# Kernel tuning notes

Measured on AMD Instinct MI355X. Metric: run time of the kernel, lower is better.

Reference implementation:

```python
import jax, jax.numpy as jnp
import numpy as np

B, S, D = 4, 2048, 1024
H = 4096          # adapter hidden dim
E = 4             # number of adapters / experts


def setup_inputs() -> dict:
    key = jax.random.key(0)
    ks = jax.random.split(key, 7)
    sd = 1.0 / np.sqrt(D)
    sh = 1.0 / np.sqrt(H)
    return {
        "x":  jax.random.normal(ks[0], (B, S, D), dtype=jnp.float32),
        "Wr": jax.random.uniform(ks[1], (D, E), minval=-sd, maxval=sd, dtype=jnp.float32),
        "br": jax.random.uniform(ks[2], (E,), minval=-sd, maxval=sd, dtype=jnp.float32),
        "W1": jax.random.uniform(ks[3], (E, D, H), minval=-sd, maxval=sd, dtype=jnp.float32),
        "b1": jax.random.uniform(ks[4], (E, H), minval=-sd, maxval=sd, dtype=jnp.float32),
        "W2": jax.random.uniform(ks[5], (E, H, D), minval=-sh, maxval=sh, dtype=jnp.float32),
        "b2": jax.random.uniform(ks[6], (E, D), minval=-sh, maxval=sh, dtype=jnp.float32),
    }


def reference(x, Wr, br, W1, b1, W2, b2):
    # Flatten tokens: (N, D)
    xf = x.reshape(-1, D)
    N = xf.shape[0]

    # Top-1 router (route_type='none' -> router input is x itself)
    logits = xf @ Wr + br                      # (N, E)
    probs = jax.nn.softmax(logits, axis=-1)    # (N, E)
    gate_idx = jnp.argmax(probs, axis=-1)      # (N,) int
    gate_val = jnp.max(probs, axis=-1)         # (N,)

    # Run every expert adapter densely (E small), then select per token.
    h = jnp.einsum('nd,edh->enh', xf, W1) + b1[:, None, :]   # (E, N, H)
    h = jax.nn.silu(h)
    eo = jnp.einsum('enh,ehd->end', h, W2) + b2[:, None, :]  # (E, N, D)

    sel = eo[gate_idx, jnp.arange(N)]          # (N, D) per-token expert output
    out = sel * gate_val[:, None]              # is_scale_prob=True scaling
    return out.reshape(B, S, D)
```

## Files before the change

### kernel.cpp

```cpp
#include <hip/hip_runtime.h>

#define DN 8192
#define DD 1024
#define DH 4096
#define DE 4
#define SLOTS (DN + 512)

typedef unsigned short u16;
typedef float f32x4 __attribute__((ext_vector_type(4)));
typedef __bf16 bf16x8 __attribute__((ext_vector_type(8)));
typedef u16 u16x2 __attribute__((ext_vector_type(2)));
typedef u16 u16x4 __attribute__((ext_vector_type(4)));

__device__ __forceinline__ u16 f2b(float f) {
  union { float f; unsigned u; } v; v.f = f;
  return (u16)((v.u + 0x7FFFu + ((v.u >> 16) & 1u)) >> 16);
}

__device__ __forceinline__ void gl_lds16(const u16* g, u16* l) {
  __builtin_amdgcn_global_load_lds((const __attribute__((address_space(1))) void*)g,
                                   (__attribute__((address_space(3))) void*)l, 16, 0, 0);
}

__global__ __launch_bounds__(256) void router_k(const float* __restrict__ x,
    const float* __restrict__ Wr, const float* __restrict__ br,
    float* __restrict__ gval, int* __restrict__ gidx, int* __restrict__ gpos,
    int* __restrict__ counts, u16* __restrict__ xb)
{
  const int tid = blockIdx.x * 256 + threadIdx.x;
  const int n = tid >> 6, lane = tid & 63;
  const float* xr = x + (size_t)n * DD;
  double a0 = 0., a1 = 0., a2 = 0., a3 = 0.;
#pragma unroll
  for (int k = 0; k < DD / 64; ++k) {
    const int d = lane + k * 64;
    const float xv = xr[d];
    const f32x4 w = *(const f32x4*)&Wr[d * 4];
    a0 += (double)xv * w[0]; a1 += (double)xv * w[1];
    a2 += (double)xv * w[2]; a3 += (double)xv * w[3];
    xb[(size_t)n * DD + d] = f2b(xv);
  }
#pragma unroll
  for (int off = 32; off; off >>= 1) {
    a0 += __shfl_xor(a0, off);
    a1 += __shfl_xor(a1, off);
    a2 += __shfl_xor(a2, off);
    a3 += __shfl_xor(a3, off);
  }
  if (lane == 0) {
    const double l0 = a0 + br[0], l1 = a1 + br[1], l2 = a2 + br[2], l3 = a3 + br[3];
    int bi = 0; double bm = l0;
    if (l1 > bm) { bm = l1; bi = 1; }
    if (l2 > bm) { bm = l2; bi = 2; }
    if (l3 > bm) { bm = l3; bi = 3; }
    const float s = __expf((float)(l0 - bm)) + __expf((float)(l1 - bm)) +
                    __expf((float)(l2 - bm)) + __expf((float)(l3 - bm));
    gval[n] = 1.0f / s;
    gidx[n] = bi;
    gpos[n] = atomicAdd(&counts[bi], 1);
  }
}

__global__ void offsets_k(const int* __restrict__ counts, int* __restrict__ offs) {
  if (threadIdx.x == 0 && blockIdx.x == 0) {
    int o = 0;
#pragma unroll
    for (int e = 0; e < DE; ++e) { offs[e] = o; o += (counts[e] + 127) & ~127; }
    offs[DE] = o;
  }
}

__global__ __launch_bounds__(256) void scatter_k(const int* __restrict__ gidx,
    const int* __restrict__ gpos, const int* __restrict__ offs, int* __restrict__ tlist) {
  const int n = blockIdx.x * 256 + threadIdx.x;
  tlist[offs[gidx[n]] + gpos[n]] = n;
}

__global__ __launch_bounds__(256) void transpose_conv(const float* __restrict__ in,
    u16* __restrict__ out, int R, int C)
{
  __shared__ u16 t[64][66];
  const int r0 = blockIdx.x * 64, c0 = blockIdx.y * 64;
  const size_t mo = (size_t)blockIdx.z * R * C;
  const int tid = threadIdx.x;
  const int i = tid >> 4, j0 = (tid & 15) * 4;
#pragma unroll
  for (int k = 0; k < 4; ++k) {
    const int row = k * 16 + i;
    const f32x4 v = *(const f32x4*)&in[mo + (size_t)(r0 + row) * C + c0 + j0];
    u16x2 u01; u01[0] = f2b(v[0]); u01[1] = f2b(v[1]);
    u16x2 u23; u23[0] = f2b(v[2]); u23[1] = f2b(v[3]);
    *(u16x2*)&t[row][j0] = u01;
    *(u16x2*)&t[row][j0 + 2] = u23;
  }
  __syncthreads();
#pragma unroll
  for (int k = 0; k < 4; ++k) {
    const int p = k * 16 + i;
    u16x4 u;
    u[0] = t[j0 + 0][p]; u[1] = t[j0 + 1][p]; u[2] = t[j0 + 2][p]; u[3] = t[j0 + 3][p];
    *(u16x4*)&out[mo + (size_t)(c0 + p) * R + r0 + j0] = u;
  }
}

__global__ __launch_bounds__(256) void gemm1_k(const u16* __restrict__ xb,
    const u16* __restrict__ w1t, const float* __restrict__ b1,
    const int* __restrict__ tlist, const int* __restrict__ offs, u16* __restrict__ hb)
{
  __shared__ u16 As[4][128][8];
  __shared__ u16 Bs[4][128][8];
  const int row0 = blockIdx.x * 128;
  if (row0 >= offs[DE]) return;
  int e = 0;
  if (row0 >= offs[1]) e = 1;
  if (row0 >= offs[2]) e = 2;
  if (row0 >= offs[3]) e = 3;
  const int h0 = blockIdx.y * 128;
  const int tid = threadIdx.x;
  const int wid = tid >> 6, lane = tid & 63;

  int tA0 = tlist[row0 + lane];
  int tA1 = tlist[row0 + 64 + lane];
  if (tA0 < 0) tA0 = 0;
  if (tA1 < 0) tA1 = 0;
  const u16* pa0 = xb + (size_t)tA0 * DD + wid * 8;
  const u16* pa1 = xb + (size_t)tA1 * DD + wid * 8;
  const u16* pb0 = w1t + (size_t)e * DH * DD + (size_t)(h0 + lane) * DD + wid * 8;
  const u16* pb1 = w1t + (size_t)e * DH * DD + (size_t)(h0 + 64 + lane) * DD + wid * 8;
  u16* lA0 = &As[wid][0][0];
  u16* lA1 = &As[wid][64][0];
  u16* lB0 = &Bs[wid][0][0];
  u16* lB1 = &Bs[wid][64][0];

  const int wr = (wid >> 1) * 64, wc = (wid & 1) * 64;
  const int fr = lane & 15, fq = lane >> 4;

  f32x4 acc[4][4];
#pragma unroll
  for (int m = 0; m < 4; ++m)
#pragma unroll
    for (int n = 0; n < 4; ++n) acc[m][n] = (f32x4)(0.f);

  for (int ks = 0; ks < DD / 32; ++ks) {
    gl_lds16(pa0, lA0); gl_lds16(pa1, lA1);
    gl_lds16(pb0, lB0); gl_lds16(pb1, lB1);
    pa0 += 32; pa1 += 32; pb0 += 32; pb1 += 32;
    __syncthreads();
    bf16x8 af[4], bfv[4];
#pragma unroll
    for (int m = 0; m < 4; ++m) af[m] = *(const bf16x8*)&As[fq][wr + m * 16 + fr][0];
#pragma unroll
    for (int n = 0; n < 4; ++n) bfv[n] = *(const bf16x8*)&Bs[fq][wc + n * 16 + fr][0];
#pragma unroll
    for (int m = 0; m < 4; ++m)
#pragma unroll
      for (int n = 0; n < 4; ++n)
        acc[m][n] = __builtin_amdgcn_mfma_f32_16x16x32_bf16(af[m], bfv[n], acc[m][n], 0, 0, 0);
    __syncthreads();
  }

#pragma unroll
  for (int n = 0; n < 4; ++n) {
    const int h = h0 + wc + n * 16 + fr;
    const float bias = b1[(size_t)e * DH + h];
#pragma unroll
    for (int m = 0; m < 4; ++m) {
      const int r = row0 + wr + m * 16 + fq * 4;
      const f32x4 v = acc[m][n];
#pragma unroll
      for (int i = 0; i < 4; ++i) {
        const float xv = v[i] + bias;
        const float sv = xv / (1.f + __expf(-xv));
        hb[(size_t)(r + i) * DH + h] = f2b(sv);
      }
    }
  }
}

__global__ __launch_bounds__(256) void gemm2_k(const u16* __restrict__ hb,
    const u16* __restrict__ w2t, const float* __restrict__ b2,
    const int* __restrict__ tlist, const int* __restrict__ offs,
    const float* __restrict__ gval, float* __restrict__ out)
{
  __shared__ u16 As[4][128][8];
  __shared__ u16 Bs[4][128][8];
  const int row0 = blockIdx.x * 128;
  if (row0 >= offs[DE]) return;
  int e = 0;
  if (row0 >= offs[1]) e = 1;
  if (row0 >= offs[2]) e = 2;
  if (row0 >= offs[3]) e = 3;
  const int d0 = blockIdx.y * 128;
  const int tid = threadIdx.x;
  const int wid = tid >> 6, lane = tid & 63;

  const u16* pa0 = hb + (size_t)(row0 + lane) * DH + wid * 8;
  const u16* pa1 = hb + (size_t)(row0 + 64 + lane) * DH + wid * 8;
  const u16* pb0 = w2t + (size_t)e * DD * DH + (size_t)(d0 + lane) * DH + wid * 8;
  const u16* pb1 = w2t + (size_t)e * DD * DH + (size_t)(d0 + 64 + lane) * DH + wid * 8;
  u16* lA0 = &As[wid][0][0];
  u16* lA1 = &As[wid][64][0];
  u16* lB0 = &Bs[wid][0][0];
  u16* lB1 = &Bs[wid][64][0];

  const int wr = (wid >> 1) * 64, wc = (wid & 1) * 64;
  const int fr = lane & 15, fq = lane >> 4;

  f32x4 acc[4][4];
#pragma unroll
  for (int m = 0; m < 4; ++m)
#pragma unroll
    for (int n = 0; n < 4; ++n) acc[m][n] = (f32x4)(0.f);

  for (int ks = 0; ks < DH / 32; ++ks) {
    gl_lds16(pa0, lA0); gl_lds16(pa1, lA1);
    gl_lds16(pb0, lB0); gl_lds16(pb1, lB1);
    pa0 += 32; pa1 += 32; pb0 += 32; pb1 += 32;
    __syncthreads();
    bf16x8 af[4], bfv[4];
#pragma unroll
    for (int m = 0; m < 4; ++m) af[m] = *(const bf16x8*)&As[fq][wr + m * 16 + fr][0];
#pragma unroll
    for (int n = 0; n < 4; ++n) bfv[n] = *(const bf16x8*)&Bs[fq][wc + n * 16 + fr][0];
#pragma unroll
    for (int m = 0; m < 4; ++m)
#pragma unroll
      for (int n = 0; n < 4; ++n)
        acc[m][n] = __builtin_amdgcn_mfma_f32_16x16x32_bf16(af[m], bfv[n], acc[m][n], 0, 0, 0);
    __syncthreads();
  }

  int tok[4][4]; float gv4[4][4];
#pragma unroll
  for (int m = 0; m < 4; ++m) {
    const int rb = row0 + wr + m * 16 + fq * 4;
#pragma unroll
    for (int i = 0; i < 4; ++i) {
      const int t = tlist[rb + i];
      tok[m][i] = t;
      gv4[m][i] = (t >= 0) ? gval[t] : 0.f;
    }
  }
#pragma unroll
  for (int n = 0; n < 4; ++n) {
    const int d = d0 + wc + n * 16 + fr;
    const float bias = b2[(size_t)e * DD + d];
#pragma unroll
    for (int m = 0; m < 4; ++m)
#pragma unroll
      for (int i = 0; i < 4; ++i) {
        const int t = tok[m][i];
        if (t >= 0) out[(size_t)t * DD + d] = (acc[m][n][i] + bias) * gv4[m][i];
      }
  }
}

extern "C" void kernel_launch(void* const* d_in, const int* in_sizes, int n_in,
                              void* d_out, int out_size, void* d_ws, size_t ws_size,
                              hipStream_t stream) {
  const float* x  = (const float*)d_in[0];
  const float* Wr = (const float*)d_in[1];
  const float* br = (const float*)d_in[2];
  const float* W1 = (const float*)d_in[3];
  const float* b1 = (const float*)d_in[4];
  const float* W2 = (const float*)d_in[5];
  const float* b2 = (const float*)d_in[6];
  float* out = (float*)d_out;

  char* ws = (char*)d_ws;
  int*   counts = (int*)ws;
  int*   offs   = (int*)(ws + 256);
  float* gval   = (float*)(ws + 512);
  int*   gidx   = (int*)(ws + 512 + 32768);
  int*   gpos   = (int*)(ws + 512 + 65536);
  int*   tlist  = (int*)(ws + 512 + 98304);
  size_t off = 512 + 98304 + 34816;
  u16* xb  = (u16*)(ws + off); off += (size_t)DN * DD * 2;
  u16* w1t = (u16*)(ws + off); off += (size_t)DE * DH * DD * 2;
  u16* w2t = (u16*)(ws + off); off += (size_t)DE * DD * DH * 2;
  u16* hb  = (u16*)(ws + off);

  hipMemsetAsync(counts, 0, 256, stream);
  hipMemsetAsync(tlist, 0xFF, SLOTS * sizeof(int), stream);

  router_k<<<dim3(DN / 4), 256, 0, stream>>>(x, Wr, br, gval, gidx, gpos, counts, xb);
  offsets_k<<<dim3(1), 64, 0, stream>>>(counts, offs);
  scatter_k<<<dim3(DN / 256), 256, 0, stream>>>(gidx, gpos, offs, tlist);
  transpose_conv<<<dim3(DD / 64, DH / 64, DE), 256, 0, stream>>>(W1, w1t, DD, DH);
  transpose_conv<<<dim3(DH / 64, DD / 64, DE), 256, 0, stream>>>(W2, w2t, DH, DD);
  gemm1_k<<<dim3(DN / 128 + DE, DH / 128), 256, 0, stream>>>(xb, w1t, b1, tlist, offs, hb);
  gemm2_k<<<dim3(DN / 128 + DE, DD / 128), 256, 0, stream>>>(hb, w2t, b2, tlist, offs, gval, out);
}
```

Measured before the change: 713.7 us.

## Double-buffer LDS in expert GEMMs and split-K the second GEMM

Both grouped GEMMs now use two LDS buffers. The next K-slice is prefetched with global_load_lds while the current slice runs through MFMA, using explicit vmcnt waits and raw barriers so loads overlap compute. gemm2 is split in two along K through a third grid dimension, which doubles the block count. The second half is written to a scratch buffer that reuses the xb/w1t workspace, and a new reduce kernel adds the halves, applies the bias and scales by the gate. The cost is an extra fp32 read/write pass over the output and one more launch.

New measurement: 677.9 us. 5.0% less time.

```diff
diff --git a/kernel.cpp b/kernel.cpp
--- a/kernel.cpp
+++ b/kernel.cpp
@@ -103,12 +103,46 @@
   }
 }
 
+#define STAGE(ks, B) do { \
+    gl_lds16(pa0 + (size_t)(ks) * 32, &As[B][wid][0][0]); \
+    gl_lds16(pa1 + (size_t)(ks) * 32, &As[B][wid][64][0]); \
+    gl_lds16(pb0 + (size_t)(ks) * 32, &Bs[B][wid][0][0]); \
+    gl_lds16(pb1 + (size_t)(ks) * 32, &Bs[B][wid][64][0]); \
+  } while (0)
+
+#define COMPUTE(B) do { \
+    bf16x8 af[4], bfv[4]; \
+    _Pragma("unroll") \
+    for (int m = 0; m < 4; ++m) af[m] = *(const bf16x8*)&As[B][fq][wr + m * 16 + fr][0]; \
+    _Pragma("unroll") \
+    for (int n = 0; n < 4; ++n) bfv[n] = *(const bf16x8*)&Bs[B][fq][wc + n * 16 + fr][0]; \
+    _Pragma("unroll") \
+    for (int m = 0; m < 4; ++m) \
+      _Pragma("unroll") \
+      for (int n = 0; n < 4; ++n) \
+        acc[m][n] = __builtin_amdgcn_mfma_f32_16x16x32_bf16(af[m], bfv[n], acc[m][n], 0, 0, 0); \
+  } while (0)
+
+#define GITER(ks, CUR, NXT, NK) do { \
+    if ((ks) + 1 < (NK)) { \
+      STAGE((ks) + 1, NXT); \
+      asm volatile("s_waitcnt vmcnt(4)" ::: "memory"); \
+    } else { \
+      asm volatile("s_waitcnt vmcnt(0)" ::: "memory"); \
+    } \
+    __builtin_amdgcn_s_barrier(); \
+    __builtin_amdgcn_sched_barrier(0); \
+    COMPUTE(CUR); \
+    __builtin_amdgcn_sched_barrier(0); \
+    __builtin_amdgcn_s_barrier(); \
+  } while (0)
+
 __global__ __launch_bounds__(256) void gemm1_k(const u16* __restrict__ xb,
     const u16* __restrict__ w1t, const float* __restrict__ b1,
     const int* __restrict__ tlist, const int* __restrict__ offs, u16* __restrict__ hb)
 {
-  __shared__ u16 As[4][128][8];
-  __shared__ u16 Bs[4][128][8];
+  __shared__ u16 As[2][4][128][8];
+  __shared__ u16 Bs[2][4][128][8];
   const int row0 = blockIdx.x * 128;
   if (row0 >= offs[DE]) return;
   int e = 0;
@@ -127,10 +161,6 @@
   const u16* pa1 = xb + (size_t)tA1 * DD + wid * 8;
   const u16* pb0 = w1t + (size_t)e * DH * DD + (size_t)(h0 + lane) * DD + wid * 8;
   const u16* pb1 = w1t + (size_t)e * DH * DD + (size_t)(h0 + 64 + lane) * DD + wid * 8;
-  u16* lA0 = &As[wid][0][0];
-  u16* lA1 = &As[wid][64][0];
-  u16* lB0 = &Bs[wid][0][0];
-  u16* lB1 = &Bs[wid][64][0];
 
   const int wr = (wid >> 1) * 64, wc = (wid & 1) * 64;
   const int fr = lane & 15, fq = lane >> 4;
@@ -141,22 +171,11 @@
 #pragma unroll
     for (int n = 0; n < 4; ++n) acc[m][n] = (f32x4)(0.f);
 
-  for (int ks = 0; ks < DD / 32; ++ks) {
-    gl_lds16(pa0, lA0); gl_lds16(pa1, lA1);
-    gl_lds16(pb0, lB0); gl_lds16(pb1, lB1);
-    pa0 += 32; pa1 += 32; pb0 += 32; pb1 += 32;
-    __syncthreads();
-    bf16x8 af[4], bfv[4];
-#pragma unroll
-    for (int m = 0; m < 4; ++m) af[m] = *(const bf16x8*)&As[fq][wr + m * 16 + fr][0];
-#pragma unroll
-    for (int n = 0; n < 4; ++n) bfv[n] = *(const bf16x8*)&Bs[fq][wc + n * 16 + fr][0];
-#pragma unroll
-    for (int m = 0; m < 4; ++m)
-#pragma unroll
-      for (int n = 0; n < 4; ++n)
-        acc[m][n] = __builtin_amdgcn_mfma_f32_16x16x32_bf16(af[m], bfv[n], acc[m][n], 0, 0, 0);
-    __syncthreads();
+  STAGE(0, 0);
+#pragma unroll 1
+  for (int ks = 0; ks < DD / 32; ks += 2) {
+    GITER(ks, 0, 1, DD / 32);
+    GITER(ks + 1, 1, 0, DD / 32);
   }
 
 #pragma unroll
@@ -178,12 +197,11 @@
 }
 
 __global__ __launch_bounds__(256) void gemm2_k(const u16* __restrict__ hb,
-    const u16* __restrict__ w2t, const float* __restrict__ b2,
-    const int* __restrict__ tlist, const int* __restrict__ offs,
-    const float* __restrict__ gval, float* __restrict__ out)
-{
-  __shared__ u16 As[4][128][8];
-  __shared__ u16 Bs[4][128][8];
+    const u16* __restrict__ w2t, const int* __restrict__ tlist,
+    const int* __restrict__ offs, float* __restrict__ out, float* __restrict__ p1)
+{
+  __shared__ u16 As[2][4][128][8];
+  __shared__ u16 Bs[2][4][128][8];
   const int row0 = blockIdx.x * 128;
   if (row0 >= offs[DE]) return;
   int e = 0;
@@ -191,17 +209,14 @@
   if (row0 >= offs[2]) e = 2;
   if (row0 >= offs[3]) e = 3;
   const int d0 = blockIdx.y * 128;
+  const int kb = blockIdx.z * (DH / 2);
   const int tid = threadIdx.x;
   const int wid = tid >> 6, lane = tid & 63;
 
-  const u16* pa0 = hb + (size_t)(row0 + lane) * DH + wid * 8;
-  const u16* pa1 = hb + (size_t)(row0 + 64 + lane) * DH + wid * 8;
-  const u16* pb0 = w2t + (size_t)e * DD * DH + (size_t)(d0 + lane) * DH + wid * 8;
-  const u16* pb1 = w2t + (size_t)e * DD * DH + (size_t)(d0 + 64 + lane) * DH + wid * 8;
-  u16* lA0 = &As[wid][0][0];
-  u16* lA1 = &As[wid][64][0];
-  u16* lB0 = &Bs[wid][0][0];
-  u16* lB1 = &Bs[wid][64][0];
+  const u16* pa0 = hb + (size_t)(row0 + lane) * DH + kb + wid * 8;
+  const u16* pa1 = hb + (size_t)(row0 + 64 + lane) * DH + kb + wid * 8;
+  const u16* pb0 = w2t + (size_t)e * DD * DH + (size_t)(d0 + lane) * DH + kb + wid * 8;
+  const u16* pb1 = w2t + (size_t)e * DD * DH + (size_t)(d0 + 64 + lane) * DH + kb + wid * 8;
 
   const int wr = (wid >> 1) * 64, wc = (wid & 1) * 64;
   const int fr = lane & 15, fq = lane >> 4;
@@ -212,47 +227,50 @@
 #pragma unroll
     for (int n = 0; n < 4; ++n) acc[m][n] = (f32x4)(0.f);
 
-  for (int ks = 0; ks < DH / 32; ++ks) {
-    gl_lds16(pa0, lA0); gl_lds16(pa1, lA1);
-    gl_lds16(pb0, lB0); gl_lds16(pb1, lB1);
-    pa0 += 32; pa1 += 32; pb0 += 32; pb1 += 32;
-    __syncthreads();
-    bf16x8 af[4], bfv[4];
-#pragma unroll
-    for (int m = 0; m < 4; ++m) af[m] = *(const bf16x8*)&As[fq][wr + m * 16 + fr][0];
-#pragma unroll
-    for (int n = 0; n < 4; ++n) bfv[n] = *(const bf16x8*)&Bs[fq][wc + n * 16 + fr][0];
-#pragma unroll
-    for (int m = 0; m < 4; ++m)
-#pragma unroll
-      for (int n = 0; n < 4; ++n)
-        acc[m][n] = __builtin_amdgcn_mfma_f32_16x16x32_bf16(af[m], bfv[n], acc[m][n], 0, 0, 0);
-    __syncthreads();
-  }
-
-  int tok[4][4]; float gv4[4][4];
+  STAGE(0, 0);
+#pragma unroll 1
+  for (int ks = 0; ks < DH / 2 / 32; ks += 2) {
+    GITER(ks, 0, 1, DH / 2 / 32);
+    GITER(ks + 1, 1, 0, DH / 2 / 32);
+  }
+
+  float* __restrict__ dst = (blockIdx.z == 0) ? out : p1;
+  int tok[4][4];
 #pragma unroll
   for (int m = 0; m < 4; ++m) {
     const int rb = row0 + wr + m * 16 + fq * 4;
 #pragma unroll
-    for (int i = 0; i < 4; ++i) {
-      const int t = tlist[rb + i];
-      tok[m][i] = t;
-      gv4[m][i] = (t >= 0) ? gval[t] : 0.f;
-    }
+    for (int i = 0; i < 4; ++i) tok[m][i] = tlist[rb + i];
   }
 #pragma unroll
   for (int n = 0; n < 4; ++n) {
     const int d = d0 + wc + n * 16 + fr;
-    const float bias = b2[(size_t)e * DD + d];
 #pragma unroll
     for (int m = 0; m < 4; ++m)
 #pragma unroll
       for (int i = 0; i < 4; ++i) {
         const int t = tok[m][i];
-        if (t >= 0) out[(size_t)t * DD + d] = (acc[m][n][i] + bias) * gv4[m][i];
+        if (t >= 0) dst[(size_t)t * DD + d] = acc[m][n][i];
       }
   }
+}
+
+__global__ __launch_bounds__(256) void reduce2_k(float* __restrict__ out,
+    const float* __restrict__ p1, const float* __restrict__ b2,
+    const int* __restrict__ gidx, const float* __restrict__ gval)
+{
+  const size_t idx = ((size_t)blockIdx.x * 256 + threadIdx.x) * 4;
+  const int n = (int)(idx >> 10);
+  const int d = (int)(idx & (DD - 1));
+  const int e = gidx[n];
+  const float g = gval[n];
+  f32x4 a = *(f32x4*)&out[idx];
+  const f32x4 b = *(const f32x4*)&p1[idx];
+  const f32x4 bb = *(const f32x4*)&b2[(size_t)e * DD + d];
+  f32x4 r;
+#pragma unroll
+  for (int j = 0; j < 4; ++j) r[j] = (a[j] + b[j] + bb[j]) * g;
+  *(f32x4*)&out[idx] = r;
 }
 
 extern "C" void kernel_launch(void* const* d_in, const int* in_sizes, int n_in,
@@ -275,7 +293,9 @@
   int*   gpos   = (int*)(ws + 512 + 65536);
   int*   tlist  = (int*)(ws + 512 + 98304);
   size_t off = 512 + 98304 + 34816;
-  u16* xb  = (u16*)(ws + off); off += (size_t)DN * DD * 2;
+  u16* xb  = (u16*)(ws + off);
+  float* p1 = (float*)(ws + off);
+  off += (size_t)DN * DD * 2;
   u16* w1t = (u16*)(ws + off); off += (size_t)DE * DH * DD * 2;
   u16* w2t = (u16*)(ws + off); off += (size_t)DE * DD * DH * 2;
   u16* hb  = (u16*)(ws + off);
@@ -289,5 +309,6 @@
   transpose_conv<<<dim3(DD / 64, DH / 64, DE), 256, 0, stream>>>(W1, w1t, DD, DH);
   transpose_conv<<<dim3(DH / 64, DD / 64, DE), 256, 0, stream>>>(W2, w2t, DH, DD);
   gemm1_k<<<dim3(DN / 128 + DE, DH / 128), 256, 0, stream>>>(xb, w1t, b1, tlist, offs, hb);
-  gemm2_k<<<dim3(DN / 128 + DE, DD / 128), 256, 0, stream>>>(hb, w2t, b2, tlist, offs, gval, out);
-}
+  gemm2_k<<<dim3(DN / 128 + DE, DD / 128, 2), 256, 0, stream>>>(hb, w2t, tlist, offs, out, p1);
+  reduce2_k<<<dim3(DN * DD / 4 / 256), 256, 0, stream>>>(out, p1, b2, gidx, gval);
+}
```
